# Kernel tuning notes

Measured on AMD Instinct MI355X. Metric: run time of the kernel, lower is better.

Reference implementation:

```python
import jax, jax.numpy as jnp
import numpy as np

N_NODES = 100000
N_EDGES = 1000000
N_GRAPHS = 512
IN_DIM = 3
HID = 64


def setup_inputs() -> dict:
    key = jax.random.key(0)
    ks = jax.random.split(key, 7)
    x = jax.random.normal(ks[0], (N_NODES, IN_DIM), dtype=jnp.float32)
    edge_index = jax.random.randint(ks[1], (2, N_EDGES), 0, N_NODES, dtype=jnp.int64)
    batch = jnp.sort(jax.random.randint(ks[2], (N_NODES,), 0, N_GRAPHS, dtype=jnp.int64))
    # Glorot-ish init for GCNConv linear weights (PyG uses glorot), zero bias.
    W1 = jax.random.normal(ks[3], (IN_DIM, HID), dtype=jnp.float32) / np.float32(np.sqrt(IN_DIM))
    b1 = jnp.zeros((HID,), dtype=jnp.float32)
    W2 = jax.random.normal(ks[4], (HID, HID), dtype=jnp.float32) / np.float32(np.sqrt(HID))
    b2 = jnp.zeros((HID,), dtype=jnp.float32)
    return {"x": x, "W1": W1, "b1": b1, "W2": W2, "b2": b2,
            "edge_index": edge_index, "batch": batch}


def reference(x, W1, b1, W2, b2, edge_index, batch):
    n = x.shape[0]
    loop = jnp.arange(n)
    # GCNConv adds self-loops, then symmetric normalization D^-1/2 (A+I) D^-1/2
    src = jnp.concatenate([edge_index[0], loop])  # [E+N]
    dst = jnp.concatenate([edge_index[1], loop])  # [E+N]
    deg = jax.ops.segment_sum(jnp.ones(dst.shape[0], x.dtype), dst, num_segments=n)
    dinv = jnp.where(deg > 0, jax.lax.rsqrt(deg), 0.0)
    norm = dinv[src] * dinv[dst]  # [E+N]

    def gcn_conv(h, W, b):
        hw = h @ W                       # [N, out] linear first (PyG order)
        msg = hw[src] * norm[:, None]    # gather + scale, [E+N, out]
        agg = jax.ops.segment_sum(msg, dst, num_segments=n)  # scatter-add
        return agg + b

    h = jax.nn.relu(gcn_conv(x, W1, b1))
    h = jax.nn.relu(gcn_conv(h, W2, b2))

    # global_mean_pool over the batch vector
    sums = jax.ops.segment_sum(h, batch, num_segments=N_GRAPHS)          # [G, HID]
    counts = jax.ops.segment_sum(jnp.ones(n, h.dtype), batch, num_segments=N_GRAPHS)
    return sums / jnp.maximum(counts, 1.0)[:, None]
```

## Files before the change

kernel.cpp:

```cpp
#include <hip/hip_runtime.h>

#define HID 64
#define N_GRAPHS_C 512
#define BSHIFT 8
#define NBUCK_MAX 512
#define CAP 3264
#define EPB 4096

typedef unsigned short u16;
typedef unsigned int u32;
typedef unsigned long long u64;

__device__ __forceinline__ float bf2f(u16 u) {
    union { u32 i; float f; } v; v.i = ((u32)u) << 16; return v.f;
}
__device__ __forceinline__ u16 f2bf(float f) {
    union { float f; u32 i; } v; v.f = f;
    u32 x = v.i;
    return (u16)((x + 0x7fffu + ((x >> 16) & 1u)) >> 16);
}


__device__ __forceinline__ int lower_bound(const int* __restrict__ a, int n, int key) {
    int lo = 0, hi = n;
    while (lo < hi) {
        int mid = (lo + hi) >> 1;
        if (a[mid] < key) lo = mid + 1; else hi = mid;
    }
    return lo;
}

__global__ void prep(int* __restrict__ gcursor, const int* __restrict__ batch,
                     int* __restrict__ gstart, int n, int nGraphs) {
    int t = threadIdx.x;
    gcursor[t] = 0;
    for (int g = t; g <= nGraphs; g += 512)
        gstart[g] = lower_bound(batch, n, g);
}


__global__ void bin_pairs(const int* __restrict__ src, const int* __restrict__ dst,
                          int* __restrict__ gcursor, u32* __restrict__ pairs,
                          int nE, int nbuck) {
    __shared__ int lh[NBUCK_MAX];
    __shared__ int lbase[NBUCK_MAX];
    int t = threadIdx.x;
    lh[t] = 0;
    __syncthreads();
    int base = blockIdx.x * EPB;
    u32 pk[8]; int rj[8], bj[8];
    #pragma unroll
    for (int j = 0; j < 8; ++j) {
        int e = base + j * 512 + t;
        if (e < nE) {
            int s = src[e], d = dst[e];
            bj[j] = d >> BSHIFT;
            pk[j] = ((u32)(d & 255) << 17) | (u32)s;
            rj[j] = atomicAdd(&lh[bj[j]], 1);
        } else {
            bj[j] = -1;
        }
    }
    __syncthreads();
    if (t < nbuck) lbase[t] = (lh[t] > 0) ? atomicAdd(&gcursor[t], lh[t]) : 0;
    __syncthreads();
    #pragma unroll
    for (int j = 0; j < 8; ++j) {
        if (bj[j] >= 0) {
            int pos = bj[j] * CAP + lbase[bj[j]] + rj[j];
            pairs[pos] = pk[j];
        }
    }
}

__global__ void build_csr(const u32* __restrict__ pairs, const int* __restrict__ gcursor,
                          int* __restrict__ csr_src, int2* __restrict__ off2,
                          float* __restrict__ dinv, const float* __restrict__ x,
                          float4* __restrict__ xs, u16* __restrict__ A16, int n) {
    __shared__ int hist[256];
    __shared__ int tmp[256];
    int t = threadIdx.x;
    int b = blockIdx.x;
    int pbeg = b * CAP;
    int pend = pbeg + gcursor[b];
    if (t < 256) hist[t] = 0;
    if (b == 0 && t < 32) ((u32*)(A16 + (size_t)n * HID))[t] = 0;
    __syncthreads();
    for (int i = pbeg + t; i < pend; i += 512)
        atomicAdd(&hist[pairs[i] >> 17], 1);
    __syncthreads();
    int v = 0;
    if (t < 256) { v = hist[t]; tmp[t] = v; }
    __syncthreads();
    for (int d = 1; d < 256; d <<= 1) {
        int add = (t >= d && t < 256) ? tmp[t - d] : 0;
        __syncthreads();
        if (t < 256) tmp[t] += add;
        __syncthreads();
    }
    if (t < 256) {
        int e = pbeg + tmp[t] - v;
        int node = (b << BSHIFT) + t;
        if (node < n) {
            float dv = rsqrtf((float)(v + 1));
            off2[node] = make_int2(e, e + v);
            dinv[node] = dv;
            xs[node] = make_float4(x[3*node]*dv, x[3*node+1]*dv, x[3*node+2]*dv, dv);
        }
        hist[t] = e;
    }
    __syncthreads();
    for (int i = pbeg + t; i < pend; i += 512) {
        u32 p = pairs[i];
        int pos = atomicAdd(&hist[p >> 17], 1);
        csr_src[pos] = (int)(p & 0x1FFFFu);
    }
}


#define MMN 128
__global__ void agg_mm2(const float4* __restrict__ xs, const int* __restrict__ csr_src,
                        const int2* __restrict__ off2,
                        const float* __restrict__ W1, const float* __restrict__ b1,
                        const float* __restrict__ W2,
                        u16* __restrict__ A16, int n) {
    __shared__ float w[HID * HID];
    __shared__ float hT[HID][MMN];
    __shared__ float dd[MMN];
    __shared__ float w1s[4 * HID];
    float4* paggs = (float4*)&hT[0][0];
    int t = threadIdx.x;

    for (int i = t; i < HID * HID; i += 256) w[i] = W2[i];
    if (t < HID) {
        w1s[t]           = W1[t];
        w1s[HID + t]     = W1[HID + t];
        w1s[2 * HID + t] = W1[2 * HID + t];
        w1s[3 * HID + t] = b1[t];
    }

    int base = blockIdx.x * MMN;
    int nl = t >> 1, half = t & 1;
    int node = base + nl;
    float a0 = 0.f, a1 = 0.f, a2 = 0.f, dv = 0.f;
    if (node < n) {
        int2 be = off2[node];
        int beg = be.x, end = be.y, e1 = end - 1;
        if (half == 0) {
            float4 self = xs[node];
            a0 = self.x; a1 = self.y; a2 = self.z; dv = self.w;
            dd[nl] = dv;
        }
        for (int k = beg + half * 8; k < end; k += 16) {
            int idx[8]; float4 v[8];
            #pragma unroll
            for (int j = 0; j < 8; ++j) idx[j] = csr_src[min(k + j, e1)];
            #pragma unroll
            for (int j = 0; j < 8; ++j) v[j] = xs[idx[j]];
            #pragma unroll
            for (int j = 0; j < 8; ++j) {
                if (k + j < end) { a0 += v[j].x; a1 += v[j].y; a2 += v[j].z; }
            }
        }
    } else if (half == 0) {
        dd[nl] = 0.f;
    }
    paggs[(nl << 1) | half] = make_float4(a0, a1, a2, dv);
    __syncthreads();

    int nl1 = t & 127;
    float4 pa = paggs[nl1 * 2], pb = paggs[nl1 * 2 + 1];
    float4 a = make_float4(pa.x + pb.x, pa.y + pb.y, pa.z + pb.z, pa.w + pb.w);
    __syncthreads();
    int fbase = t >> 7;
    #pragma unroll
    for (int s = 0; s < 32; ++s) {
        int f = fbase + 2 * s;
        float v = (a.x * w1s[f] + a.y * w1s[HID + f] + a.z * w1s[2 * HID + f]) * a.w
                  + w1s[3 * HID + f];
        hT[f][nl1] = v > 0.f ? v : 0.f;
    }
    __syncthreads();

    int fq = t & 15, oct = t >> 4;
    int nb = oct * 8;
    float acc[8][4];
    #pragma unroll
    for (int j = 0; j < 8; ++j)
        #pragma unroll
        for (int q = 0; q < 4; ++q) acc[j][q] = 0.f;

    #pragma unroll 4
    for (int k = 0; k < HID; ++k) {
        float4 w4 = *(const float4*)&w[k * HID + fq * 4];
        float4 h0 = *(const float4*)&hT[k][nb];
        float4 h1 = *(const float4*)&hT[k][nb + 4];
        float hv[8] = { h0.x, h0.y, h0.z, h0.w, h1.x, h1.y, h1.z, h1.w };
        #pragma unroll
        for (int j = 0; j < 8; ++j) {
            acc[j][0] += hv[j] * w4.x;
            acc[j][1] += hv[j] * w4.y;
            acc[j][2] += hv[j] * w4.z;
            acc[j][3] += hv[j] * w4.w;
        }
    }

    #pragma unroll
    for (int j = 0; j < 8; ++j) {
        int nodej = base + nb + j;
        if (nodej < n) {
            float dj = dd[nb + j];
            u64 outp = (u64)f2bf(acc[j][0] * dj)
                     | ((u64)f2bf(acc[j][1] * dj) << 16)
                     | ((u64)f2bf(acc[j][2] * dj) << 32)
                     | ((u64)f2bf(acc[j][3] * dj) << 48);
            *(u64*)(A16 + ((size_t)nodej << 6) + (fq << 2)) = outp;
        }
    }
}


__global__ void gather_nodes(const u16* __restrict__ A16, const float* __restrict__ dinv,
                             const int* __restrict__ csr_src, const int2* __restrict__ off2,
                             const float* __restrict__ bias,
                             u16* __restrict__ H16, int n) {
    int t = threadIdx.x;
    int waveq = t >> 4;
    int m = t & 15;
    int qbase = t & 48;
    int node = blockIdx.x * 16 + waveq;
    if (node >= n) return;
    int2 be = off2[node];
    int beg = be.x, end = be.y;
    u64 selfrow = *(const u64*)(A16 + ((size_t)node << 6) + (m << 2));
    u32 slo = (u32)selfrow, shi = (u32)(selfrow >> 32);
    float acc0 = bf2f((u16)(slo & 0xffffu));
    float acc1 = bf2f((u16)(slo >> 16));
    float acc2 = bf2f((u16)(shi & 0xffffu));
    float acc3 = bf2f((u16)(shi >> 16));
    const char* Ab = (const char*)A16;
    u32 laneoff = (u32)(m << 3);
    for (int k = beg; k < end; k += 8) {
        int lim = min(end - k, 8);
        int myIdx = (m < lim) ? csr_src[k + m] : n;
        int ss[8]; u64 rows[8];
        #pragma unroll
        for (int j = 0; j < 8; ++j)
            ss[j] = __shfl(myIdx, qbase + j, 64);
        #pragma unroll
        for (int j = 0; j < 8; ++j)
            rows[j] = *(const u64*)(Ab + (((u32)ss[j] << 7) | laneoff));
        #pragma unroll
        for (int j = 0; j < 8; ++j) {
            u32 lo = (u32)rows[j], hi = (u32)(rows[j] >> 32);
            acc0 += bf2f((u16)(lo & 0xffffu));
            acc1 += bf2f((u16)(lo >> 16));
            acc2 += bf2f((u16)(hi & 0xffffu));
            acc3 += bf2f((u16)(hi >> 16));
        }
    }
    float ddv = dinv[node];
    float4 bb = *(const float4*)(bias + (m << 2));
    float v0 = fmaxf(acc0 * ddv + bb.x, 0.0f);
    float v1 = fmaxf(acc1 * ddv + bb.y, 0.0f);
    float v2 = fmaxf(acc2 * ddv + bb.z, 0.0f);
    float v3 = fmaxf(acc3 * ddv + bb.w, 0.0f);
    u64 outp = (u64)f2bf(v0) | ((u64)f2bf(v1) << 16)
             | ((u64)f2bf(v2) << 32) | ((u64)f2bf(v3) << 48);
    *(u64*)(H16 + ((size_t)node << 6) + (m << 2)) = outp;
}


__global__ void pool_graph(const u16* __restrict__ H16, const int* __restrict__ gstart,
                           float* __restrict__ out, int n) {
    int g = blockIdx.x;
    int t = threadIdx.x;
    int lo = gstart[g];
    int hi = gstart[g + 1];
    int cntN = hi - lo;
    int sid = t >> 4;
    int m = t & 15;
    float a0 = 0.f, a1 = 0.f, a2 = 0.f, a3 = 0.f;
    int i = lo + sid;
    for (; i + 16 < hi; i += 32) {
        u64 r0 = *(const u64*)(H16 + ((size_t)i << 6) + (m << 2));
        u64 r1 = *(const u64*)(H16 + ((size_t)(i + 16) << 6) + (m << 2));
        u32 l0 = (u32)r0, h0 = (u32)(r0 >> 32);
        u32 l1 = (u32)r1, h1 = (u32)(r1 >> 32);
        a0 += bf2f((u16)(l0 & 0xffffu)) + bf2f((u16)(l1 & 0xffffu));
        a1 += bf2f((u16)(l0 >> 16))     + bf2f((u16)(l1 >> 16));
        a2 += bf2f((u16)(h0 & 0xffffu)) + bf2f((u16)(h1 & 0xffffu));
        a3 += bf2f((u16)(h0 >> 16))     + bf2f((u16)(h1 >> 16));
    }
    if (i < hi) {
        u64 r0 = *(const u64*)(H16 + ((size_t)i << 6) + (m << 2));
        u32 l0 = (u32)r0, h0 = (u32)(r0 >> 32);
        a0 += bf2f((u16)(l0 & 0xffffu));
        a1 += bf2f((u16)(l0 >> 16));
        a2 += bf2f((u16)(h0 & 0xffffu));
        a3 += bf2f((u16)(h0 >> 16));
    }
    a0 += __shfl_xor(a0, 16, 64); a0 += __shfl_xor(a0, 32, 64);
    a1 += __shfl_xor(a1, 16, 64); a1 += __shfl_xor(a1, 32, 64);
    a2 += __shfl_xor(a2, 16, 64); a2 += __shfl_xor(a2, 32, 64);
    a3 += __shfl_xor(a3, 16, 64); a3 += __shfl_xor(a3, 32, 64);
    __shared__ float smf[4 * HID];
    int wave = t >> 6, lane = t & 63;
    if (lane < 16) {
        smf[wave * HID + 4 * lane + 0] = a0;
        smf[wave * HID + 4 * lane + 1] = a1;
        smf[wave * HID + 4 * lane + 2] = a2;
        smf[wave * HID + 4 * lane + 3] = a3;
    }
    __syncthreads();
    if (t < HID) {
        float s = smf[t] + smf[HID + t] + smf[2 * HID + t] + smf[3 * HID + t];
        out[(size_t)g * HID + t] = s / fmaxf((float)cntN, 1.0f);
    }
}


extern "C" void kernel_launch(void* const* d_in, const int* in_sizes, int n_in,
                              void* d_out, int out_size, void* d_ws, size_t ws_size,
                              hipStream_t stream) {
    const float* x  = (const float*)d_in[0];
    const float* W1 = (const float*)d_in[1];
    const float* b1 = (const float*)d_in[2];
    const float* W2 = (const float*)d_in[3];
    const float* b2 = (const float*)d_in[4];
    const int*   ei = (const int*)d_in[5];
    const int*   batch = (const int*)d_in[6];

    const int n  = in_sizes[0] / 3;
    const int nE = in_sizes[5] / 2;
    const int* src = ei;
    const int* dst = ei + nE;
    const int nbuck = (n + ((1 << BSHIFT) - 1)) >> BSHIFT;
    const int nGraphs = out_size / HID;

    char* p = (char*)d_ws;
    int*    gcursor = (int*)p;                p += 2048;
    int*    gstart  = (int*)p;                p += 4096;
    int*    csr_src = (int*)p;                p += (size_t)nbuck * CAP * 4;
    int2*   off2    = (int2*)p;               p += (size_t)n * 8;
    float*  dinv    = (float*)p;              p += (size_t)n * 4;
    float4* xs      = (float4*)p;             p += (size_t)n * 16;
    u16*    A16     = (u16*)p;                p += (size_t)(n + 1) * HID * 2;
    u16*    H2      = (u16*)p;                p += (size_t)n * HID * 2;
    u32*    pairs   = (u32*)A16;

    const int gridE2   = (nE + EPB - 1) / EPB;
    const int gridMM2  = (n + MMN - 1) / MMN;
    const int gridGath = (n + 15) / 16;
    const int BT = 256;

    prep<<<1, 512, 0, stream>>>(gcursor, batch, gstart, n, nGraphs);
    bin_pairs<<<gridE2, 512, 0, stream>>>(src, dst, gcursor, pairs, nE, nbuck);
    build_csr<<<nbuck, 512, 0, stream>>>(pairs, gcursor, csr_src, off2, dinv, x, xs, A16, n);

    agg_mm2<<<gridMM2, BT, 0, stream>>>(xs, csr_src, off2, W1, b1, W2, A16, n);

    gather_nodes<<<gridGath, BT, 0, stream>>>(A16, dinv, csr_src, off2, b2, H2, n);

    pool_graph<<<nGraphs, BT, 0, stream>>>(H2, gstart, (float*)d_out, n);
}
```

Baseline: 157.2 us.

## Fuse mean pooling into second-layer gather with atomic accumulation

Merges the second GCN gather and the global mean pool into one kernel. Each node's ReLU output is pre-scaled by 1/count and added straight into the output with atomics, using a block-level reduction when all 16 nodes in a block belong to the same graph. This removes the intermediate H buffer write/read and one kernel launch. The prep kernel is replaced by a memset, with gstart computation and output zeroing moved into build_csr blocks 0 and 1. In exchange it adds float atomics to the output and a batch lookup per node.

```diff
diff --git a/kernel.cpp b/kernel.cpp
--- a/kernel.cpp
+++ b/kernel.cpp
@@ -20,7 +20,6 @@
     return (u16)((x + 0x7fffu + ((x >> 16) & 1u)) >> 16);
 }
 
-
 __device__ __forceinline__ int lower_bound(const int* __restrict__ a, int n, int key) {
     int lo = 0, hi = n;
     while (lo < hi) {
@@ -28,14 +27,6 @@
         if (a[mid] < key) lo = mid + 1; else hi = mid;
     }
     return lo;
-}
-
-__global__ void prep(int* __restrict__ gcursor, const int* __restrict__ batch,
-                     int* __restrict__ gstart, int n, int nGraphs) {
-    int t = threadIdx.x;
-    gcursor[t] = 0;
-    for (int g = t; g <= nGraphs; g += 512)
-        gstart[g] = lower_bound(batch, n, g);
 }
 
 
@@ -76,7 +67,9 @@
 __global__ void build_csr(const u32* __restrict__ pairs, const int* __restrict__ gcursor,
                           int* __restrict__ csr_src, int2* __restrict__ off2,
                           float* __restrict__ dinv, const float* __restrict__ x,
-                          float4* __restrict__ xs, u16* __restrict__ A16, int n) {
+                          float4* __restrict__ xs, u16* __restrict__ A16,
+                          const int* __restrict__ batch, int* __restrict__ gstart,
+                          float* __restrict__ out, int nGraphs, int n) {
     __shared__ int hist[256];
     __shared__ int tmp[256];
     int t = threadIdx.x;
@@ -85,6 +78,15 @@
     int pend = pbeg + gcursor[b];
     if (t < 256) hist[t] = 0;
     if (b == 0 && t < 32) ((u32*)(A16 + (size_t)n * HID))[t] = 0;
+    if (b == 0) {
+        for (int g = t; g <= nGraphs; g += 512)
+            gstart[g] = lower_bound(batch, n, g);
+    }
+    if (b == 1) {
+        float4* o4 = (float4*)out;
+        int tot = nGraphs * HID / 4;
+        for (int i = t; i < tot; i += 512) o4[i] = make_float4(0.f, 0.f, 0.f, 0.f);
+    }
     __syncthreads();
     for (int i = pbeg + t; i < pend; i += 512)
         atomicAdd(&hist[pairs[i] >> 17], 1);
@@ -220,19 +222,27 @@
 }
 
 
-__global__ void gather_nodes(const u16* __restrict__ A16, const float* __restrict__ dinv,
-                             const int* __restrict__ csr_src, const int2* __restrict__ off2,
-                             const float* __restrict__ bias,
-                             u16* __restrict__ H16, int n) {
+__global__ void gather_pool(const u16* __restrict__ A16, const float* __restrict__ dinv,
+                            const int* __restrict__ csr_src, const int2* __restrict__ off2,
+                            const float* __restrict__ bias, const int* __restrict__ batch,
+                            const int* __restrict__ gstart, float* __restrict__ out,
+                            int n) {
+    __shared__ float smw[4 * HID];
+    __shared__ int sgmin, sgmax;
     int t = threadIdx.x;
+    if (t == 0) { sgmin = 0x7fffffff; sgmax = -1; }
     int waveq = t >> 4;
     int m = t & 15;
     int qbase = t & 48;
     int node = blockIdx.x * 16 + waveq;
-    if (node >= n) return;
-    int2 be = off2[node];
-    int beg = be.x, end = be.y;
-    u64 selfrow = *(const u64*)(A16 + ((size_t)node << 6) + (m << 2));
+    bool valid = (node < n);
+    int g = batch[valid ? node : (n - 1)];
+    __syncthreads();
+    if (m == 0) { atomicMin(&sgmin, g); atomicMax(&sgmax, g); }
+
+    int beg = 0, end = 0;
+    if (valid) { int2 be = off2[node]; beg = be.x; end = be.y; }
+    u64 selfrow = *(const u64*)(A16 + ((size_t)(valid ? node : n) << 6) + (m << 2));
     u32 slo = (u32)selfrow, shi = (u32)(selfrow >> 32);
     float acc0 = bf2f((u16)(slo & 0xffffu));
     float acc1 = bf2f((u16)(slo >> 16));
@@ -259,63 +269,40 @@
             acc3 += bf2f((u16)(hi >> 16));
         }
     }
-    float ddv = dinv[node];
+    float ddv = valid ? dinv[node] : 0.f;
+    int cnt = gstart[g + 1] - gstart[g];
+    float inv = valid ? (1.0f / fmaxf((float)cnt, 1.0f)) : 0.f;
     float4 bb = *(const float4*)(bias + (m << 2));
-    float v0 = fmaxf(acc0 * ddv + bb.x, 0.0f);
-    float v1 = fmaxf(acc1 * ddv + bb.y, 0.0f);
-    float v2 = fmaxf(acc2 * ddv + bb.z, 0.0f);
-    float v3 = fmaxf(acc3 * ddv + bb.w, 0.0f);
-    u64 outp = (u64)f2bf(v0) | ((u64)f2bf(v1) << 16)
-             | ((u64)f2bf(v2) << 32) | ((u64)f2bf(v3) << 48);
-    *(u64*)(H16 + ((size_t)node << 6) + (m << 2)) = outp;
-}
-
-
-__global__ void pool_graph(const u16* __restrict__ H16, const int* __restrict__ gstart,
-                           float* __restrict__ out, int n) {
-    int g = blockIdx.x;
-    int t = threadIdx.x;
-    int lo = gstart[g];
-    int hi = gstart[g + 1];
-    int cntN = hi - lo;
-    int sid = t >> 4;
-    int m = t & 15;
-    float a0 = 0.f, a1 = 0.f, a2 = 0.f, a3 = 0.f;
-    int i = lo + sid;
-    for (; i + 16 < hi; i += 32) {
-        u64 r0 = *(const u64*)(H16 + ((size_t)i << 6) + (m << 2));
-        u64 r1 = *(const u64*)(H16 + ((size_t)(i + 16) << 6) + (m << 2));
-        u32 l0 = (u32)r0, h0 = (u32)(r0 >> 32);
-        u32 l1 = (u32)r1, h1 = (u32)(r1 >> 32);
-        a0 += bf2f((u16)(l0 & 0xffffu)) + bf2f((u16)(l1 & 0xffffu));
-        a1 += bf2f((u16)(l0 >> 16))     + bf2f((u16)(l1 >> 16));
-        a2 += bf2f((u16)(h0 & 0xffffu)) + bf2f((u16)(h1 & 0xffffu));
-        a3 += bf2f((u16)(h0 >> 16))     + bf2f((u16)(h1 >> 16));
-    }
-    if (i < hi) {
-        u64 r0 = *(const u64*)(H16 + ((size_t)i << 6) + (m << 2));
-        u32 l0 = (u32)r0, h0 = (u32)(r0 >> 32);
-        a0 += bf2f((u16)(l0 & 0xffffu));
-        a1 += bf2f((u16)(l0 >> 16));
-        a2 += bf2f((u16)(h0 & 0xffffu));
-        a3 += bf2f((u16)(h0 >> 16));
-    }
-    a0 += __shfl_xor(a0, 16, 64); a0 += __shfl_xor(a0, 32, 64);
-    a1 += __shfl_xor(a1, 16, 64); a1 += __shfl_xor(a1, 32, 64);
-    a2 += __shfl_xor(a2, 16, 64); a2 += __shfl_xor(a2, 32, 64);
-    a3 += __shfl_xor(a3, 16, 64); a3 += __shfl_xor(a3, 32, 64);
-    __shared__ float smf[4 * HID];
-    int wave = t >> 6, lane = t & 63;
-    if (lane < 16) {
-        smf[wave * HID + 4 * lane + 0] = a0;
-        smf[wave * HID + 4 * lane + 1] = a1;
-        smf[wave * HID + 4 * lane + 2] = a2;
-        smf[wave * HID + 4 * lane + 3] = a3;
-    }
-    __syncthreads();
-    if (t < HID) {
-        float s = smf[t] + smf[HID + t] + smf[2 * HID + t] + smf[3 * HID + t];
-        out[(size_t)g * HID + t] = s / fmaxf((float)cntN, 1.0f);
+    float v0 = fmaxf(acc0 * ddv + bb.x, 0.0f) * inv;
+    float v1 = fmaxf(acc1 * ddv + bb.y, 0.0f) * inv;
+    float v2 = fmaxf(acc2 * ddv + bb.z, 0.0f) * inv;
+    float v3 = fmaxf(acc3 * ddv + bb.w, 0.0f) * inv;
+
+    __syncthreads();
+    if (sgmin == sgmax) {
+        v0 += __shfl_xor(v0, 16, 64); v0 += __shfl_xor(v0, 32, 64);
+        v1 += __shfl_xor(v1, 16, 64); v1 += __shfl_xor(v1, 32, 64);
+        v2 += __shfl_xor(v2, 16, 64); v2 += __shfl_xor(v2, 32, 64);
+        v3 += __shfl_xor(v3, 16, 64); v3 += __shfl_xor(v3, 32, 64);
+        int wave = t >> 6, lane = t & 63;
+        if (lane < 16) {
+            smw[wave * HID + 4 * lane + 0] = v0;
+            smw[wave * HID + 4 * lane + 1] = v1;
+            smw[wave * HID + 4 * lane + 2] = v2;
+            smw[wave * HID + 4 * lane + 3] = v3;
+        }
+        __syncthreads();
+        if (t < HID) {
+            float s = smw[t] + smw[HID + t] + smw[2 * HID + t] + smw[3 * HID + t];
+            atomicAdd(&out[(size_t)sgmin * HID + t], s);
+        }
+    } else {
+        if (valid) {
+            atomicAdd(&out[(size_t)g * HID + 4 * m + 0], v0);
+            atomicAdd(&out[(size_t)g * HID + 4 * m + 1], v1);
+            atomicAdd(&out[(size_t)g * HID + 4 * m + 2], v2);
+            atomicAdd(&out[(size_t)g * HID + 4 * m + 3], v3);
+        }
     }
 }
 
@@ -346,7 +333,6 @@
     float*  dinv    = (float*)p;              p += (size_t)n * 4;
     float4* xs      = (float4*)p;             p += (size_t)n * 16;
     u16*    A16     = (u16*)p;                p += (size_t)(n + 1) * HID * 2;
-    u16*    H2      = (u16*)p;                p += (size_t)n * HID * 2;
     u32*    pairs   = (u32*)A16;
 
     const int gridE2   = (nE + EPB - 1) / EPB;
@@ -354,13 +340,13 @@
     const int gridGath = (n + 15) / 16;
     const int BT = 256;
 
-    prep<<<1, 512, 0, stream>>>(gcursor, batch, gstart, n, nGraphs);
+    hipMemsetAsync(gcursor, 0, 2048, stream);
     bin_pairs<<<gridE2, 512, 0, stream>>>(src, dst, gcursor, pairs, nE, nbuck);
-    build_csr<<<nbuck, 512, 0, stream>>>(pairs, gcursor, csr_src, off2, dinv, x, xs, A16, n);
+    build_csr<<<nbuck, 512, 0, stream>>>(pairs, gcursor, csr_src, off2, dinv, x, xs,
+                                         A16, batch, gstart, (float*)d_out, nGraphs, n);
 
     agg_mm2<<<gridMM2, BT, 0, stream>>>(xs, csr_src, off2, W1, b1, W2, A16, n);
 
-    gather_nodes<<<gridGath, BT, 0, stream>>>(A16, dinv, csr_src, off2, b2, H2, n);
-
-    pool_graph<<<nGraphs, BT, 0, stream>>>(H2, gstart, (float*)d_out, n);
-}
+    gather_pool<<<gridGath, BT, 0, stream>>>(A16, dinv, csr_src, off2, b2,
+                                             batch, gstart, (float*)d_out, n);
+}
```

Result: slower. 161.6 us (+2.8%).
